# Kernel tuning notes

Measured on AMD Instinct MI355X. Metric: run time of the kernel, lower is better.

## Reference

```python
import jax, jax.numpy as jnp
import numpy as np

B = 65536        # batch_size
F = 128          # feature_dim (shared-layer output)
H = 256          # hidden dim of each domain tower
D = 8            # num_domains
OUT = 1          # per-domain tower output dim


def setup_inputs() -> dict:
    key = jax.random.key(0)
    k_x, k_w1, k_b1, k_w2, k_b2, k_id = jax.random.split(key, 6)
    x = jax.random.normal(k_x, (B, F), dtype=jnp.float32)
    select_domain_ids = jax.random.randint(k_id, (B,), 0, D)
    # stacked per-domain MLP params (one tower per domain)
    s1 = 1.0 / np.sqrt(F)
    s2 = 1.0 / np.sqrt(H)
    W1 = jax.random.uniform(k_w1, (D, F, H), minval=-s1, maxval=s1, dtype=jnp.float32)
    b1 = jax.random.uniform(k_b1, (D, H), minval=-s1, maxval=s1, dtype=jnp.float32)
    W2 = jax.random.uniform(k_w2, (D, H, OUT), minval=-s2, maxval=s2, dtype=jnp.float32)
    b2 = jax.random.uniform(k_b2, (D, OUT), minval=-s2, maxval=s2, dtype=jnp.float32)
    return {"x": x, "select_domain_ids": select_domain_ids,
            "W1": W1, "b1": b1, "W2": W2, "b2": b2}


def reference(x, select_domain_ids, W1, b1, W2, b2):
    # Run EVERY domain tower on the full batch (dense compute), as the
    # original module does, then gather the selected domain per sample.
    h = jax.nn.relu(jnp.einsum('bf,dfh->bdh', x, W1) + b1)      # [B, D, H]
    logits = jnp.einsum('bdh,dho->bdo', h, W2) + b2             # [B, D, OUT]
    # domain_select: logits[arange(B), domain_ids] -> [B, OUT]
    out = jnp.take_along_axis(logits, select_domain_ids[:, None, None], axis=1)[:, 0]
    return out
```

## Files before the change

### kernel.cpp

```cpp
#include <hip/hip_runtime.h>
#include <hip/hip_bf16.h>

#define BN 65536
#define FD 128
#define HD 256
#define DN 8
#define NB 256
#define TM 64
#define GRID_MAIN 1024

typedef float f32x4 __attribute__((ext_vector_type(4)));
using bf16x8 = __attribute__((ext_vector_type(8))) __bf16;
typedef unsigned short us4 __attribute__((ext_vector_type(4)));

__device__ __forceinline__ unsigned short f2bf(float f) {
  unsigned int x = __float_as_uint(f);
  x += 0x7fffu + ((x >> 16) & 1u);
  return (unsigned short)(x >> 16);
}

__global__ __launch_bounds__(256) void kA(
    const float* __restrict__ W1, const int* __restrict__ ids,
    unsigned short* __restrict__ W1T, int* __restrict__ cnt_blk) {
  __shared__ int hist[DN];
  __shared__ unsigned short tile[64][136];
  int t = threadIdx.x, bid = blockIdx.x;
  if (bid < NB) {
    if (t < DN) hist[t] = 0;
    __syncthreads();
    atomicAdd(&hist[ids[bid * 256 + t]], 1);
    __syncthreads();
    if (t < DN) cnt_blk[bid * DN + t] = hist[t];
  } else {
    int db = (bid - NB) >> 2, hb = (bid - NB) & 3;
    int fr = t >> 4, hq = t & 15;
    const float* src = W1 + (size_t)db * FD * HD + hb * 64 + hq * 4;
#pragma unroll
    for (int jj = 0; jj < 8; jj++) {
      int f = fr + 16 * jj;
      f32x4 v = *(const f32x4*)(src + (size_t)f * HD);
#pragma unroll
      for (int e = 0; e < 4; e++) tile[hq * 4 + e][f] = f2bf(v[e]);
    }
    __syncthreads();
    unsigned short* dst = W1T + (size_t)db * HD * FD + (size_t)hb * 64 * FD;
    int h = t >> 2, c = t & 3;
#pragma unroll
    for (int j = 0; j < 4; j++) {
      int f = c * 32 + j * 8;
      *(us4*)(dst + h * FD + f)     = *(const us4*)&tile[h][f];
      *(us4*)(dst + h * FD + f + 4) = *(const us4*)&tile[h][f + 4];
    }
  }
}

__global__ __launch_bounds__(512) void kB(
    const int* __restrict__ cnt_blk, int* __restrict__ blk_base,
    int* __restrict__ g_cnt, int* __restrict__ tile_list,
    int* __restrict__ n_tiles) {
  __shared__ int s_cnt[DN], s_T[DN + 1];
  int t = threadIdx.x, d = t >> 6, l = t & 63;
  int c[4], sum = 0;
#pragma unroll
  for (int j = 0; j < 4; j++) { c[j] = cnt_blk[(l * 4 + j) * DN + d]; sum += c[j]; }
  int run = sum;
  for (int off = 1; off < 64; off <<= 1) {
    int v = __shfl_up(run, off);
    if (l >= off) run += v;
  }
  int excl = run - sum;
#pragma unroll
  for (int j = 0; j < 4; j++) { blk_base[(l * 4 + j) * DN + d] = excl; excl += c[j]; }
  if (l == 63) s_cnt[d] = run;
  __syncthreads();
  if (t == 0) {
    int T = 0;
    for (int dd = 0; dd < DN; dd++) {
      g_cnt[dd] = s_cnt[dd];
      s_T[dd] = T;
      T += (s_cnt[dd] + TM - 1) / TM;
    }
    s_T[DN] = T;
    *n_tiles = T;
  }
  __syncthreads();
  int T = s_T[DN];
  for (int tt = t; tt < T; tt += 512) {
    int dd = 0;
    while (s_T[dd + 1] <= tt) dd++;
    tile_list[tt] = dd | ((tt - s_T[dd]) << 3);
  }
}

__global__ __launch_bounds__(256) void kC(
    const int* __restrict__ ids, const int* __restrict__ blk_base,
    int* __restrict__ perm) {
  __shared__ int hist[DN], base[DN];
  int t = threadIdx.x, bid = blockIdx.x;
  if (t < DN) { hist[t] = 0; base[t] = (t << 16) + blk_base[bid * DN + t]; }
  __syncthreads();
  int i = bid * 256 + t;
  int id = ids[i];
  int lp = atomicAdd(&hist[id], 1);
  perm[base[id] + lp] = i;
}

__global__ __launch_bounds__(512, 4) void kmain(
    const float* __restrict__ x, const float* __restrict__ b1,
    const float* __restrict__ W2, const float* __restrict__ b2,
    const unsigned short* __restrict__ W1T, const int* __restrict__ perm,
    const int* __restrict__ g_cnt, const int* __restrict__ tile_list,
    const int* __restrict__ n_tiles, float* __restrict__ out) {
  __shared__ unsigned short xs[TM * FD];
  __shared__ float s_red[TM][9];
  int T = *n_tiles;
  int t = threadIdx.x;
  int lane = t & 63, w = t >> 6;
  int lg = lane >> 4, lr = lane & 15;

  for (int i = blockIdx.x; i < T; i += GRID_MAIN) {
    int info = tile_list[i];
    int d = info & 7, k = info >> 3;
    int rows = min(g_cnt[d] - k * TM, TM);
    const int* pr = perm + (d << 16) + k * TM;
    const unsigned short* Wd = W1T + (size_t)d * HD * FD;

    float b1v[2], w2v[2];
    bf16x8 bfr[4][2];
#pragma unroll
    for (int nt = 0; nt < 2; nt++) {
      int col = w * 32 + nt * 16 + lr;
      b1v[nt] = b1[d * HD + col];
      w2v[nt] = W2[d * HD + col];
#pragma unroll
      for (int ks = 0; ks < 4; ks++)
        bfr[ks][nt] = *(const bf16x8*)(Wd + (size_t)col * FD + ks * 32 + lg * 8);
    }

    {
      int r = t >> 3, c8 = t & 7;
      int gi = pr[min(r, rows - 1)];
      const float* xr = x + (size_t)gi * FD;
      f32x4 v[4];
#pragma unroll
      for (int j = 0; j < 4; j++) v[j] = *(const f32x4*)(xr + (c8 + 8 * j) * 4);
#pragma unroll
      for (int j = 0; j < 4; j++) {
        int fc = c8 + 8 * j;
        int us = (r * FD + fc * 4) ^ ((r & 7) << 3);
        us4 wv;
        wv[0] = f2bf(v[j][0]); wv[1] = f2bf(v[j][1]);
        wv[2] = f2bf(v[j][2]); wv[3] = f2bf(v[j][3]);
        *(us4*)&xs[us] = wv;
      }
    }
    __syncthreads();

    f32x4 acc[4][2];
#pragma unroll
    for (int mf = 0; mf < 4; mf++)
#pragma unroll
      for (int nt = 0; nt < 2; nt++) acc[mf][nt] = (f32x4){0.f, 0.f, 0.f, 0.f};

#pragma unroll
    for (int ks = 0; ks < 4; ks++) {
      bf16x8 a[4];
#pragma unroll
      for (int mf = 0; mf < 4; mf++) {
        int row = mf * 16 + lr;
        int us = (row * FD + ks * 32 + lg * 8) ^ ((row & 7) << 3);
        a[mf] = *(const bf16x8*)&xs[us];
      }
#pragma unroll
      for (int nt = 0; nt < 2; nt++)
#pragma unroll
        for (int mf = 0; mf < 4; mf++)
          acc[mf][nt] = __builtin_amdgcn_mfma_f32_16x16x32_bf16(a[mf], bfr[ks][nt], acc[mf][nt], 0, 0, 0);
    }

    float part[4][4];
#pragma unroll
    for (int mf = 0; mf < 4; mf++)
#pragma unroll
      for (int q = 0; q < 4; q++) part[mf][q] = 0.f;
#pragma unroll
    for (int nt = 0; nt < 2; nt++)
#pragma unroll
      for (int mf = 0; mf < 4; mf++)
#pragma unroll
        for (int q = 0; q < 4; q++) {
          float h = acc[mf][nt][q] + b1v[nt];
          h = h > 0.f ? h : 0.f;
          part[mf][q] = fmaf(h, w2v[nt], part[mf][q]);
        }
#pragma unroll
    for (int off = 1; off < 16; off <<= 1)
#pragma unroll
      for (int mf = 0; mf < 4; mf++)
#pragma unroll
        for (int q = 0; q < 4; q++)
          part[mf][q] += __shfl_xor(part[mf][q], off);
    if (lr == 0) {
#pragma unroll
      for (int mf = 0; mf < 4; mf++)
#pragma unroll
        for (int q = 0; q < 4; q++)
          s_red[mf * 16 + lg * 4 + q][w] = part[mf][q];
    }
    __syncthreads();
    if (t < rows) {
      const float* sr = s_red[t];
      out[pr[t]] = sr[0] + sr[1] + sr[2] + sr[3] + sr[4] + sr[5] + sr[6] + sr[7]
                   + b2[d];
    }
    __syncthreads();
  }
}

extern "C" void kernel_launch(void* const* d_in, const int* in_sizes, int n_in,
                              void* d_out, int out_size, void* d_ws, size_t ws_size,
                              hipStream_t stream) {
  const float* x   = (const float*)d_in[0];
  const int*   ids = (const int*)d_in[1];
  const float* W1  = (const float*)d_in[2];
  const float* b1  = (const float*)d_in[3];
  const float* W2  = (const float*)d_in[4];
  const float* b2  = (const float*)d_in[5];
  float* out = (float*)d_out;

  int* ws_i = (int*)d_ws;
  int* g_cnt     = ws_i;
  int* n_tiles   = ws_i + 16;
  int* cnt_blk   = ws_i + 64;
  int* blk_base  = ws_i + 2112;
  int* tile_list = ws_i + 4160;
  int* perm      = ws_i + 8192;
  unsigned short* W1T = (unsigned short*)(ws_i + 8192 + DN * BN);

  hipLaunchKernelGGL(kA, dim3(NB + 32), dim3(256), 0, stream, W1, ids, W1T, cnt_blk);
  hipLaunchKernelGGL(kB, dim3(1), dim3(512), 0, stream, cnt_blk, blk_base, g_cnt,
                     tile_list, n_tiles);
  hipLaunchKernelGGL(kC, dim3(NB), dim3(256), 0, stream, ids, blk_base, perm);
  hipLaunchKernelGGL(kmain, dim3(GRID_MAIN), dim3(512), 0, stream, x, b1, W2, b2,
                     W1T, perm, g_cnt, tile_list, n_tiles, out);
}
```

Measured before the change: 102.7 us.

## Fuse scan and scatter kernels, replace tile list with fixed domain slots

```diff
diff --git a/kernel.cpp b/kernel.cpp
--- a/kernel.cpp
+++ b/kernel.cpp
@@ -7,6 +7,7 @@
 #define DN 8
 #define NB 256
 #define TM 64
+#define SLOTS 8192
 #define GRID_MAIN 1024
 
 typedef float f32x4 __attribute__((ext_vector_type(4)));
@@ -54,74 +55,54 @@
   }
 }
 
-__global__ __launch_bounds__(512) void kB(
-    const int* __restrict__ cnt_blk, int* __restrict__ blk_base,
-    int* __restrict__ g_cnt, int* __restrict__ tile_list,
-    int* __restrict__ n_tiles) {
-  __shared__ int s_cnt[DN], s_T[DN + 1];
-  int t = threadIdx.x, d = t >> 6, l = t & 63;
-  int c[4], sum = 0;
-#pragma unroll
-  for (int j = 0; j < 4; j++) { c[j] = cnt_blk[(l * 4 + j) * DN + d]; sum += c[j]; }
-  int run = sum;
+__global__ __launch_bounds__(256) void kBC(
+    const int* __restrict__ ids, const int* __restrict__ cnt_blk,
+    int* __restrict__ g_cnt, int* __restrict__ perm) {
+  __shared__ int s_before[DN], s_total[DN], hist[DN];
+  int t = threadIdx.x, bid = blockIdx.x;
+  int w = t >> 6, l = t & 63;
+  int full0 = 0, full1 = 0, bef0 = 0, bef1 = 0;
+#pragma unroll
+  for (int j = 0; j < 4; j++) {
+    int r = l * 4 + j;
+    int2 v = *(const int2*)(cnt_blk + r * DN + 2 * w);
+    full0 += v.x; full1 += v.y;
+    if (r < bid) { bef0 += v.x; bef1 += v.y; }
+  }
+#pragma unroll
   for (int off = 1; off < 64; off <<= 1) {
-    int v = __shfl_up(run, off);
-    if (l >= off) run += v;
-  }
-  int excl = run - sum;
-#pragma unroll
-  for (int j = 0; j < 4; j++) { blk_base[(l * 4 + j) * DN + d] = excl; excl += c[j]; }
-  if (l == 63) s_cnt[d] = run;
-  __syncthreads();
-  if (t == 0) {
-    int T = 0;
-    for (int dd = 0; dd < DN; dd++) {
-      g_cnt[dd] = s_cnt[dd];
-      s_T[dd] = T;
-      T += (s_cnt[dd] + TM - 1) / TM;
-    }
-    s_T[DN] = T;
-    *n_tiles = T;
-  }
-  __syncthreads();
-  int T = s_T[DN];
-  for (int tt = t; tt < T; tt += 512) {
-    int dd = 0;
-    while (s_T[dd + 1] <= tt) dd++;
-    tile_list[tt] = dd | ((tt - s_T[dd]) << 3);
-  }
-}
-
-__global__ __launch_bounds__(256) void kC(
-    const int* __restrict__ ids, const int* __restrict__ blk_base,
-    int* __restrict__ perm) {
-  __shared__ int hist[DN], base[DN];
-  int t = threadIdx.x, bid = blockIdx.x;
-  if (t < DN) { hist[t] = 0; base[t] = (t << 16) + blk_base[bid * DN + t]; }
+    full0 += __shfl_xor(full0, off); full1 += __shfl_xor(full1, off);
+    bef0  += __shfl_xor(bef0, off);  bef1  += __shfl_xor(bef1, off);
+  }
+  if (t < DN) hist[t] = 0;
+  if (l == 0) {
+    s_before[2 * w] = bef0; s_before[2 * w + 1] = bef1;
+    s_total[2 * w] = full0; s_total[2 * w + 1] = full1;
+  }
   __syncthreads();
   int i = bid * 256 + t;
   int id = ids[i];
   int lp = atomicAdd(&hist[id], 1);
-  perm[base[id] + lp] = i;
+  perm[(id << 16) + s_before[id] + lp] = i;
+  if (bid == 0 && t < DN) g_cnt[t] = s_total[t];
 }
 
 __global__ __launch_bounds__(512, 4) void kmain(
     const float* __restrict__ x, const float* __restrict__ b1,
     const float* __restrict__ W2, const float* __restrict__ b2,
     const unsigned short* __restrict__ W1T, const int* __restrict__ perm,
-    const int* __restrict__ g_cnt, const int* __restrict__ tile_list,
-    const int* __restrict__ n_tiles, float* __restrict__ out) {
+    const int* __restrict__ g_cnt, float* __restrict__ out) {
   __shared__ unsigned short xs[TM * FD];
   __shared__ float s_red[TM][9];
-  int T = *n_tiles;
   int t = threadIdx.x;
   int lane = t & 63, w = t >> 6;
   int lg = lane >> 4, lr = lane & 15;
 
-  for (int i = blockIdx.x; i < T; i += GRID_MAIN) {
-    int info = tile_list[i];
-    int d = info & 7, k = info >> 3;
-    int rows = min(g_cnt[d] - k * TM, TM);
+  for (int s = blockIdx.x; s < SLOTS; s += GRID_MAIN) {
+    int d = s & 7, k = s >> 3;
+    int rows = g_cnt[d] - k * TM;
+    if (rows <= 0) continue;
+    rows = min(rows, TM);
     const int* pr = perm + (d << 16) + k * TM;
     const unsigned short* Wd = W1T + (size_t)d * HD * FD;
 
@@ -229,18 +210,13 @@
   float* out = (float*)d_out;
 
   int* ws_i = (int*)d_ws;
-  int* g_cnt     = ws_i;
-  int* n_tiles   = ws_i + 16;
-  int* cnt_blk   = ws_i + 64;
-  int* blk_base  = ws_i + 2112;
-  int* tile_list = ws_i + 4160;
-  int* perm      = ws_i + 8192;
-  unsigned short* W1T = (unsigned short*)(ws_i + 8192 + DN * BN);
+  int* cnt_blk = ws_i;
+  int* g_cnt   = ws_i + 2048;
+  int* perm    = ws_i + 4096;
+  unsigned short* W1T = (unsigned short*)(ws_i + 4096 + DN * BN);
 
   hipLaunchKernelGGL(kA, dim3(NB + 32), dim3(256), 0, stream, W1, ids, W1T, cnt_blk);
-  hipLaunchKernelGGL(kB, dim3(1), dim3(512), 0, stream, cnt_blk, blk_base, g_cnt,
-                     tile_list, n_tiles);
-  hipLaunchKernelGGL(kC, dim3(NB), dim3(256), 0, stream, ids, blk_base, perm);
+  hipLaunchKernelGGL(kBC, dim3(NB), dim3(256), 0, stream, ids, cnt_blk, g_cnt, perm);
   hipLaunchKernelGGL(kmain, dim3(GRID_MAIN), dim3(512), 0, stream, x, b1, W2, b2,
-                     W1T, perm, g_cnt, tile_list, n_tiles, out);
-}
+                     W1T, perm, g_cnt, out);
+}
```

After: 100.1 us. -2.6%, faster.
